# Optimization experiments

Measured on AMD Instinct MI355X. Metric: run time of the kernel, lower is better.

## Reference

```python
import jax, jax.numpy as jnp
import numpy as np

N = 100000   # nodes
E = 800000   # edges
NC = 500     # category nodes
EC = 20000   # category relation edges
D = 64       # out_feats
HOUR_PERIOD = 6  # emb_mix('hour') uses time_period = 6


def l2norm(x):
    # torch F.normalize(p=2, dim=-1) with eps clamp
    return x / jnp.maximum(jnp.linalg.norm(x, axis=-1, keepdims=True), 1e-12)


def proj_transh(x, norm):
    # x - <x, norm> * norm  (per-row)
    return x - jnp.sum(x * norm, axis=-1, keepdims=True) * norm


def edge_softmax(score, dst, n):
    # softmax over incoming edges of each destination node
    m = jax.ops.segment_max(score, dst, num_segments=n)
    e = jnp.exp(score - m[dst])
    s = jax.ops.segment_sum(e, dst, num_segments=n)
    return e / s[dst]


def setup_inputs() -> dict:
    key = jax.random.key(0)
    ks = jax.random.split(key, 12)
    nfeat = jax.random.normal(ks[0], (N, D), dtype=jnp.float32)
    cat_embedding = jax.random.normal(ks[1], (NC, D), dtype=jnp.float32)
    src = jax.random.randint(ks[2], (E,), 0, N, dtype=jnp.int32)
    dst = jax.random.randint(ks[3], (E,), 0, N, dtype=jnp.int32)
    feats_type = jax.random.randint(ks[4], (E,), 0, 7, dtype=jnp.int32)
    hour_id = jax.random.randint(ks[5], (E,), 0, HOUR_PERIOD, dtype=jnp.int32)
    cat_src = jax.random.randint(ks[6], (EC,), 0, NC, dtype=jnp.int32)
    cat_dst = jax.random.randint(ks[7], (EC,), 0, NC, dtype=jnp.int32)
    # learned parameters (embeddings are L2-normalized at init, as in torch code)
    rel_emb = l2norm(jax.random.normal(ks[8], (7, D), dtype=jnp.float32))
    norm_emb = l2norm(jax.random.normal(ks[9], (7, D), dtype=jnp.float32))
    hour_emb = l2norm(jax.random.normal(ks[10], (25, D), dtype=jnp.float32))
    time_rel_w = jax.random.normal(ks[11], (D, D), dtype=jnp.float32) * (1.0 / np.sqrt(D))
    time_rel_b = jnp.zeros((D,), dtype=jnp.float32)
    return {
        "nfeat": nfeat, "cat_embedding": cat_embedding,
        "rel_emb": rel_emb, "norm_emb": norm_emb, "hour_emb": hour_emb,
        "time_rel_w": time_rel_w, "time_rel_b": time_rel_b,
        "src": src, "dst": dst, "feats_type": feats_type, "hour_id": hour_id,
        "cat_src": cat_src, "cat_dst": cat_dst,
    }


def reference(nfeat, cat_embedding, rel_emb, norm_emb, hour_emb,
              time_rel_w, time_rel_b,
              src, dst, feats_type, hour_id, cat_src, cat_dst):
    # ---- category relation graph (cat_emb_type='relation', cat_score_type='transe')
    h_c = cat_embedding[cat_src]                        # [EC, D]
    t_c = cat_embedding[cat_dst]                        # [EC, D]
    rel_c = rel_emb[6]                                  # [D]
    diff_c = h_c + rel_c - t_c
    score_c = jnp.exp(-jnp.sum(diff_c * diff_c, axis=1))  # [EC]
    a_c = edge_softmax(score_c, cat_dst, NC)
    cat_hid = jax.ops.segment_sum(h_c * a_c[:, None], cat_dst, num_segments=NC)

    # ---- main graph edge features
    rel = rel_emb[feats_type]                           # [E, D]
    norm = norm_emb[feats_type]                         # [E, D]
    time_norm = norm_emb[5]                             # [D] (type-5 for all edges)
    # time relation: mixed hour embedding -> linear -> L2 normalize
    last_h = (hour_id - 1 + HOUR_PERIOD) % HOUR_PERIOD
    next_h = (hour_id + 1) % HOUR_PERIOD
    mix = (hour_emb[last_h] + hour_emb[hour_id] + hour_emb[next_h]) / 3.0  # [E, D]
    time_rel = l2norm(mix @ time_rel_w.T + time_rel_b)  # [E, D]

    h = nfeat[src]                                      # [E, D]
    t = nfeat[dst]                                      # [E, D]
    # TransH score on relation hyperplane
    d1 = proj_transh(h, norm) + rel - proj_transh(t, norm)
    score = jnp.exp(-jnp.sum(d1 * d1, axis=1))
    # TransH score on time hyperplane
    d2 = proj_transh(h, time_norm[None, :]) + time_rel - proj_transh(t, time_norm[None, :])
    score_t = jnp.exp(-jnp.sum(d2 * d2, axis=1))
    fin_score = score * score_t                         # [E]

    a = edge_softmax(fin_score, dst, N)                 # [E]
    rst = jax.ops.segment_sum(h * a[:, None], dst, num_segments=N)  # [N, D]
    return rst, cat_hid
```

## Files before the change

### kernel.cpp

```cpp
#include <hip/hip_runtime.h>

#define D 64
#define HOUR_PERIOD 6
#define CAPM 40
#define CAPC 96
#define CSTR 8

__device__ __forceinline__ float bf2f(unsigned short u) {
    union { unsigned int i; float f; } v; v.i = ((unsigned int)u) << 16; return v.f;
}
__device__ __forceinline__ unsigned short f2bf(float f) {
    union { float fl; unsigned int i; } v; v.fl = f;
    unsigned int x = v.i;
    return (unsigned short)((x + 0x7fffu + ((x >> 16) & 1u)) >> 16);
}
__device__ __forceinline__ float4 ld4(const void* base, int idx4, int fp32) {
    if (fp32) return reinterpret_cast<const float4*>(base)[idx4];
    ushort4 u = reinterpret_cast<const ushort4*>(base)[idx4];
    return make_float4(bf2f(u.x), bf2f(u.y), bf2f(u.z), bf2f(u.w));
}
__device__ __forceinline__ float ld1(const void* base, int i, int fp32) {
    return fp32 ? reinterpret_cast<const float*>(base)[i]
                : bf2f(reinterpret_cast<const unsigned short*>(base)[i]);
}
__device__ __forceinline__ void ld8(const void* base, int row, int l, int f,
                                    float& h0, float& h1, float& h2, float& h3,
                                    float& h4, float& h5, float& h6, float& h7) {
    if (f) {
        const float4* p = reinterpret_cast<const float4*>(base) + row * 16 + l * 2;
        float4 u = p[0], v = p[1];
        h0 = u.x; h1 = u.y; h2 = u.z; h3 = u.w;
        h4 = v.x; h5 = v.y; h6 = v.z; h7 = v.w;
    } else {
        uint4 u = reinterpret_cast<const uint4*>(base)[row * 8 + l];
        h0 = bf2f((unsigned short)(u.x & 0xFFFFu)); h1 = bf2f((unsigned short)(u.x >> 16));
        h2 = bf2f((unsigned short)(u.y & 0xFFFFu)); h3 = bf2f((unsigned short)(u.y >> 16));
        h4 = bf2f((unsigned short)(u.z & 0xFFFFu)); h5 = bf2f((unsigned short)(u.z >> 16));
        h6 = bf2f((unsigned short)(u.w & 0xFFFFu)); h7 = bf2f((unsigned short)(u.w >> 16));
    }
}
__device__ __forceinline__ int detect_f(const void* rel_emb) {
    int lane = threadIdx.x & 63;
    float da = bf2f(reinterpret_cast<const unsigned short*>(rel_emb)[lane]);
    float db = bf2f(reinterpret_cast<const unsigned short*>(rel_emb)[lane + 64]);
    int bad = (!(fabsf(da) <= 100.f)) || (!(fabsf(db) <= 100.f));
    unsigned long long m = __ballot(bad);
    return (m != 0ull) ? 1 : 0;
}
__device__ __forceinline__ float wsum64(float v) {
    #pragma unroll
    for (int off = 32; off; off >>= 1) v += __shfl_xor(v, off, 64);
    return v;
}
__device__ __forceinline__ float rsum8(float v) {
    v += __shfl_xor(v, 1, 64);
    v += __shfl_xor(v, 2, 64);
    v += __shfl_xor(v, 4, 64);
    return v;
}

__global__ void k_pp(const int* __restrict__ src, const int* __restrict__ dst,
                     const int* __restrict__ ft, const int* __restrict__ hh,
                     const int* __restrict__ csrc, const int* __restrict__ cdst,
                     int* __restrict__ cnt, unsigned* __restrict__ recsM,
                     unsigned* __restrict__ recsC,
                     const void* __restrict__ nfeat, const void* __restrict__ cemb,
                     const void* __restrict__ rel_emb, const void* __restrict__ norm_emb,
                     const void* __restrict__ hour_emb, const void* __restrict__ trw,
                     const void* __restrict__ trb,
                     unsigned* __restrict__ pmain, float2* __restrict__ pcat,
                     float* __restrict__ consts,
                     int E, int EC, int N, int NC, int GPREP) {
    __shared__ float vt[20 * D];
    __shared__ float mix6[HOUR_PERIOD * D];
    int t = threadIdx.x;
    if (blockIdx.x >= GPREP) {
        int tid = (blockIdx.x - GPREP) * 256 + t;
        if (tid < E) {
            int sv = src[tid], dv = dst[tid], fv = ft[tid], hv = hh[tid];
            int r = atomicAdd(&cnt[dv * CSTR], 1);
            if (r < CAPM)
                recsM[dv * CAPM + r] =
                    (unsigned)sv | ((unsigned)fv << 17) | ((unsigned)hv << 20);
        } else if (tid - E < EC) {
            int k = tid - E;
            int sv = csrc[k], dv = cdst[k];
            int r = atomicAdd(&cnt[(N + dv) * CSTR], 1);
            if (r < CAPC) recsC[dv * CAPC + r] = (unsigned)sv;
        }
        return;
    }
    int pb = blockIdx.x;
    int f = detect_f(rel_emb);
    int lane = t & 63, w = t >> 6;
    for (int i = t; i < 7 * D; i += 256) vt[i] = ld1(rel_emb, i, f);
    for (int i = t; i < 7 * D; i += 256) vt[7 * D + i] = ld1(norm_emb, i, f);
    for (int i = t; i < HOUR_PERIOD * D; i += 256) {
        int hv = i >> 6, k = i & 63;
        int last = (hv + HOUR_PERIOD - 1) % HOUR_PERIOD, next = (hv + 1) % HOUR_PERIOD;
        mix6[i] = (ld1(hour_emb, last * D + k, f) + ld1(hour_emb, hv * D + k, f) +
                   ld1(hour_emb, next * D + k, f)) * (1.f / 3.f);
    }
    __syncthreads();
    for (int hv = w; hv < HOUR_PERIOD; hv += 4) {
        float y = ld1(trb, lane, f);
        #pragma unroll 4
        for (int kk = 0; kk < D; ++kk)
            y += mix6[hv * D + kk] * ld1(trw, lane * D + kk, f);
        float ss = wsum64(y * y);
        vt[(14 + hv) * D + lane] = y / fmaxf(sqrtf(ss), 1e-12f);
    }
    __syncthreads();
    int tid = pb * 256 + t;
    if (tid < N) {
        float R0 = 0.f, R1 = 0.f, R2a = 0.f, R3 = 0.f, R4 = 0.f, R5 = 0.f, R6 = 0.f;
        float Nm0 = 0.f, Nm1 = 0.f, Nm2 = 0.f, Nm3 = 0.f, Nm4 = 0.f, Nm5 = 0.f, Nm6 = 0.f;
        float T0 = 0.f, T1 = 0.f, T2 = 0.f, T3 = 0.f, T4 = 0.f, T5 = 0.f;
        float S2 = 0.f;
        const float4* vp = reinterpret_cast<const float4*>(vt);
        #pragma unroll 2
        for (int k4 = 0; k4 < 16; ++k4) {
            float4 x = ld4(nfeat, tid * 16 + k4, f);
            #define DOTV(acc, v) { float4 qv = vp[(v) * 16 + k4]; \
                acc += x.x * qv.x + x.y * qv.y + x.z * qv.z + x.w * qv.w; }
            DOTV(R0, 0)  DOTV(R1, 1)  DOTV(R2a, 2) DOTV(R3, 3)
            DOTV(R4, 4)  DOTV(R5, 5)  DOTV(R6, 6)
            DOTV(Nm0, 7) DOTV(Nm1, 8) DOTV(Nm2, 9) DOTV(Nm3, 10)
            DOTV(Nm4, 11) DOTV(Nm5, 12) DOTV(Nm6, 13)
            DOTV(T0, 14) DOTV(T1, 15) DOTV(T2, 16) DOTV(T3, 17)
            DOTV(T4, 18) DOTV(T5, 19)
            #undef DOTV
            S2 += x.x * x.x + x.y * x.y + x.z * x.z + x.w * x.w;
        }
        unsigned w0 = (unsigned)f2bf(Nm0) | ((unsigned)f2bf(R0) << 16);
        unsigned w1 = (unsigned)f2bf(Nm1) | ((unsigned)f2bf(R1) << 16);
        unsigned w2 = (unsigned)f2bf(Nm2) | ((unsigned)f2bf(R2a) << 16);
        unsigned w3 = (unsigned)f2bf(Nm3) | ((unsigned)f2bf(R3) << 16);
        unsigned w4 = (unsigned)f2bf(Nm4) | ((unsigned)f2bf(R4) << 16);
        unsigned w5 = (unsigned)f2bf(Nm5) | ((unsigned)f2bf(R5) << 16);
        unsigned w6 = (unsigned)f2bf(Nm6) | ((unsigned)f2bf(R6) << 16);
        unsigned w7 = (unsigned)f2bf(T0) | ((unsigned)f2bf(T1) << 16);
        unsigned w8 = (unsigned)f2bf(T2) | ((unsigned)f2bf(T3) << 16);
        unsigned w9 = (unsigned)f2bf(T4) | ((unsigned)f2bf(T5) << 16);
        union { float ff; unsigned u; } cs, ca;
        cs.ff = S2; ca.ff = Nm5;
        uint4* dp = reinterpret_cast<uint4*>(pmain + (size_t)tid * 16);
        dp[0] = make_uint4(w0, w1, w2, w3);
        dp[1] = make_uint4(w4, w5, w6, w7);
        dp[2] = make_uint4(w8, w9, cs.u, ca.u);
        dp[3] = make_uint4(0, 0, 0, 0);
    } else if (tid - N < NC) {
        int i = tid - N;
        float S = 0.f, Cr = 0.f;
        #pragma unroll 4
        for (int k4 = 0; k4 < 16; ++k4) {
            float4 x = ld4(cemb, i * 16 + k4, f);
            float4 rv = *reinterpret_cast<const float4*>(&vt[6 * D + k4 * 4]);
            S  += x.x * x.x + x.y * x.y + x.z * x.z + x.w * x.w;
            Cr += x.x * rv.x + x.y * rv.y + x.z * rv.z + x.w * rv.w;
        }
        pcat[i] = make_float2(S, Cr);
    }
    if (pb == 0) {
        if (t < 7) {
            float R2 = 0.f, RN = 0.f, N2 = 0.f;
            for (int k = 0; k < D; ++k) {
                float r = vt[t * D + k], n = vt[(7 + t) * D + k];
                R2 += r * r; RN += r * n; N2 += n * n;
            }
            consts[t * 4 + 0] = R2; consts[t * 4 + 1] = RN;
            consts[t * 4 + 2] = N2 - 2.f; consts[t * 4 + 3] = 0.f;
        } else if (t < 13) {
            int hv = t - 7;
            float T2c = 0.f, TQ = 0.f;
            for (int k = 0; k < D; ++k) {
                float a = vt[(14 + hv) * D + k], qv = vt[12 * D + k];
                T2c += a * a; TQ += a * qv;
            }
            consts[28 + hv * 2] = T2c; consts[29 + hv * 2] = TQ;
        } else if (t == 13) {
            float Q2 = 0.f;
            for (int k = 0; k < D; ++k) { float qv = vt[12 * D + k]; Q2 += qv * qv; }
            consts[40] = Q2 - 2.f;
        } else if (t == 14) {
            float R = 0.f;
            for (int k = 0; k < D; ++k) { float r = vt[6 * D + k]; R += r * r; }
            consts[41] = R;
        }
    }
}

__launch_bounds__(256, 8)
__global__ void k_fused(const void* __restrict__ nfeat, const void* __restrict__ cemb,
                        const void* __restrict__ rel_emb,
                        const unsigned char* __restrict__ pmain,
                        const float2* __restrict__ pcat,
                        const float* __restrict__ consts,
                        const int* __restrict__ cnt,
                        const unsigned* __restrict__ recsM,
                        const unsigned* __restrict__ recsC,
                        void* __restrict__ out, int N, int M) {
    int t = threadIdx.x;
    int f = detect_f(rel_emb);
    __shared__ __align__(16) float sc[44];
    if (t < 42) sc[t] = consts[t];
    __syncthreads();
    int lane = t & 63, w = t >> 6;
    int l = lane & 7, q = lane >> 3;
    int d = blockIdx.x * 4 + w;
    if (d >= M) return;
    float Q2m2 = sc[40], R2c = sc[41];
    float a0 = 0.f, a1 = 0.f, a2 = 0.f, a3 = 0.f;
    float a4 = 0.f, a5 = 0.f, a6 = 0.f, a7 = 0.f, se = 0.f;
    if (d < N) {
        int i0 = d * CAPM;
        int nE = cnt[d * CSTR];
        unsigned pk = recsM[i0 + q];
        float t0, t1, t2, t3, t4, t5, t6, t7;
        ld8(nfeat, d, l, f, t0, t1, t2, t3, t4, t5, t6, t7);
        const unsigned char* pd = pmain + (size_t)d * 64;
        float2 sd2 = *reinterpret_cast<const float2*>(pd + 40);
        nE = nE > CAPM ? CAPM : nE;
        for (int b = 0; b < nE; b += 8) {
            unsigned pkn = 0u;
            if (b + 8 < nE) pkn = recsM[i0 + b + 8 + q];
            int valid = (b + q) < nE;
            unsigned pkv = valid ? pk : 0u;
            int s = pkv & 0x1FFFF, fv = (pkv >> 17) & 7, hv = (pkv >> 20) & 7;
            const unsigned char* ps = pmain + (size_t)s * 64;
            float h0, h1, h2, h3, h4, h5, h6, h7;
            ld8(nfeat, s, l, f, h0, h1, h2, h3, h4, h5, h6, h7);
            unsigned aws = *reinterpret_cast<const unsigned*>(ps + 4 * fv);
            unsigned short dhs = *reinterpret_cast<const unsigned short*>(ps + 28 + 2 * hv);
            float2 sa = *reinterpret_cast<const float2*>(ps + 40);
            unsigned awd = *reinterpret_cast<const unsigned*>(pd + 4 * fv);
            unsigned short dhd = *reinterpret_cast<const unsigned short*>(pd + 28 + 2 * hv);
            float4 cf  = *reinterpret_cast<float4*>(&sc[fv * 4]);
            float2 cth = *reinterpret_cast<float2*>(&sc[28 + hv * 2]);
            float hdot = rsum8(h0 * t0 + h1 * t1 + h2 * t2 + h3 * t3 +
                               h4 * t4 + h5 * t5 + h6 * t6 + h7 * t7);
            float As = bf2f((unsigned short)(aws & 0xFFFFu));
            float Cs = bf2f((unsigned short)(aws >> 16));
            float Ad = bf2f((unsigned short)(awd & 0xFFFFu));
            float Cd = bf2f((unsigned short)(awd >> 16));
            float Dhs = bf2f(dhs), Dhd = bf2f(dhd);
            float al = As - Ad;
            float be = sa.y - sd2.y;
            float w2 = sa.x + sd2.x - 2.f * hdot;
            float ssq = 2.f * w2 + cf.x + cth.x + 2.f * (Cs - Cd) + 2.f * (Dhs - Dhd)
                      + al * al * cf.z - 2.f * al * cf.y
                      + be * be * Q2m2 - 2.f * be * cth.y;
            float es = __expf(__expf(-ssq));
            es = valid ? es : 0.f;
            a0 += es * h0; a1 += es * h1; a2 += es * h2; a3 += es * h3;
            a4 += es * h4; a5 += es * h5; a6 += es * h6; a7 += es * h7;
            se += es;
            pk = pkn;
        }
    } else {
        int dc = d - N;
        int i0 = dc * CAPC;
        int nE = cnt[d * CSTR];
        unsigned pk = recsC[i0 + q];
        float t0, t1, t2, t3, t4, t5, t6, t7;
        ld8(cemb, dc, l, f, t0, t1, t2, t3, t4, t5, t6, t7);
        float2 td = pcat[dc];
        nE = nE > CAPC ? CAPC : nE;
        for (int b = 0; b < nE; b += 8) {
            unsigned pkn = 0u;
            if (b + 8 < nE) pkn = recsC[i0 + b + 8 + q];
            int valid = (b + q) < nE;
            unsigned s = valid ? pk : 0u;
            float h0, h1, h2, h3, h4, h5, h6, h7;
            ld8(cemb, (int)s, l, f, h0, h1, h2, h3, h4, h5, h6, h7);
            float2 csh = pcat[s];
            float hdot = rsum8(h0 * t0 + h1 * t1 + h2 * t2 + h3 * t3 +
                               h4 * t4 + h5 * t5 + h6 * t6 + h7 * t7);
            float ssq = csh.x + td.x + R2c + 2.f * csh.y - 2.f * td.y - 2.f * hdot;
            float es = __expf(__expf(-ssq));
            es = valid ? es : 0.f;
            a0 += es * h0; a1 += es * h1; a2 += es * h2; a3 += es * h3;
            a4 += es * h4; a5 += es * h5; a6 += es * h6; a7 += es * h7;
            se += es;
            pk = pkn;
        }
    }
    #define RED(x) x += __shfl_xor(x, 8, 64); x += __shfl_xor(x, 16, 64); x += __shfl_xor(x, 32, 64);
    RED(a0) RED(a1) RED(a2) RED(a3) RED(a4) RED(a5) RED(a6) RED(a7) RED(se)
    #undef RED
    float inv = (se > 0.f) ? 1.f / se : 0.f;
    if (q == 0) {
        if (f) {
            float4* op = reinterpret_cast<float4*>(out) + d * 16 + l * 2;
            op[0] = make_float4(a0 * inv, a1 * inv, a2 * inv, a3 * inv);
            op[1] = make_float4(a4 * inv, a5 * inv, a6 * inv, a7 * inv);
        } else {
            unsigned w0 = (unsigned)f2bf(a0 * inv) | ((unsigned)f2bf(a1 * inv) << 16);
            unsigned w1 = (unsigned)f2bf(a2 * inv) | ((unsigned)f2bf(a3 * inv) << 16);
            unsigned w2 = (unsigned)f2bf(a4 * inv) | ((unsigned)f2bf(a5 * inv) << 16);
            unsigned w3 = (unsigned)f2bf(a6 * inv) | ((unsigned)f2bf(a7 * inv) << 16);
            reinterpret_cast<uint4*>(out)[d * 8 + l] = make_uint4(w0, w1, w2, w3);
        }
    }
}

extern "C" void kernel_launch(void* const* d_in, const int* in_sizes, int n_in,
                              void* d_out, int out_size, void* d_ws, size_t ws_size,
                              hipStream_t stream) {
    const void* nfeat    = d_in[0];
    const void* cemb     = d_in[1];
    const void* rel_emb  = d_in[2];
    const void* norm_emb = d_in[3];
    const void* hour_emb = d_in[4];
    const void* trw      = d_in[5];
    const void* trb      = d_in[6];
    const int* src    = (const int*)d_in[7];
    const int* dst    = (const int*)d_in[8];
    const int* ftype  = (const int*)d_in[9];
    const int* hourid = (const int*)d_in[10];
    const int* csrc   = (const int*)d_in[11];
    const int* cdst   = (const int*)d_in[12];

    const int N  = in_sizes[0] / D;
    const int NC = in_sizes[1] / D;
    const int E  = in_sizes[7];
    const int EC = in_sizes[11];
    const int M  = N + NC;

    unsigned char* base = (unsigned char*)d_ws;
    size_t o = 0;
    int* cnt = (int*)(base + o);          o += ((size_t)M * CSTR * 4 + 255) & ~(size_t)255;
    float* consts = (float*)(base + o);   o += 256;
    unsigned* pmain = (unsigned*)(base + o); o += (size_t)N * 64;
    float2* pcat = (float2*)(base + o);   o += ((size_t)NC * 8 + 255) & ~(size_t)255;
    unsigned* recsM = (unsigned*)(base + o); o += (size_t)N * CAPM * 4;
    unsigned* recsC = (unsigned*)(base + o); o += (size_t)NC * CAPC * 4;

    (void)hipMemsetAsync(cnt, 0, (size_t)M * CSTR * 4, stream);

    int GP    = (E + EC + 255) / 256;
    int GPREP = (M + 255) / 256;
    k_pp<<<GPREP + GP, 256, 0, stream>>>(src, dst, ftype, hourid, csrc, cdst,
                                         cnt, recsM, recsC,
                                         nfeat, cemb, rel_emb, norm_emb,
                                         hour_emb, trw, trb,
                                         pmain, pcat, consts,
                                         E, EC, N, NC, GPREP);
    k_fused<<<(M + 3) / 4, 256, 0, stream>>>(nfeat, cemb, rel_emb,
                                             (const unsigned char*)pmain, pcat,
                                             consts, cnt,
                                             recsM, recsC, d_out, N, M);
}
```

Baseline: 213.3 us.

## Merge preprocessing and aggregation kernels into one persistent kernel with grid barrier

Replaces the two kernel launches with a single persistent kernel sized to the device's occupancy. Blocks grid-stride over the preprocessing and bucketing units, meet at a global atomic barrier, then grid-stride over destination nodes for aggregation. This removes one launch and the gap between kernels. In exchange, every block waits for the slowest block at the barrier, and the per-unit table setup now runs in every prep unit a block handles. The barrier deadlocks if the grid is larger than what can be co-resident on the device.

```diff
diff --git a/kernel.cpp b/kernel.cpp
--- a/kernel.cpp
+++ b/kernel.cpp
@@ -59,247 +59,253 @@
     return v;
 }
 
-__global__ void k_pp(const int* __restrict__ src, const int* __restrict__ dst,
-                     const int* __restrict__ ft, const int* __restrict__ hh,
-                     const int* __restrict__ csrc, const int* __restrict__ cdst,
-                     int* __restrict__ cnt, unsigned* __restrict__ recsM,
-                     unsigned* __restrict__ recsC,
-                     const void* __restrict__ nfeat, const void* __restrict__ cemb,
-                     const void* __restrict__ rel_emb, const void* __restrict__ norm_emb,
-                     const void* __restrict__ hour_emb, const void* __restrict__ trw,
-                     const void* __restrict__ trb,
-                     unsigned* __restrict__ pmain, float2* __restrict__ pcat,
-                     float* __restrict__ consts,
-                     int E, int EC, int N, int NC, int GPREP) {
+__global__ __launch_bounds__(256, 8) void k_mega(
+        const int* __restrict__ src, const int* __restrict__ dst,
+        const int* __restrict__ ft, const int* __restrict__ hh,
+        const int* __restrict__ csrc, const int* __restrict__ cdst,
+        int* __restrict__ cnt, unsigned* __restrict__ recsM,
+        unsigned* __restrict__ recsC,
+        const void* __restrict__ nfeat, const void* __restrict__ cemb,
+        const void* __restrict__ rel_emb, const void* __restrict__ norm_emb,
+        const void* __restrict__ hour_emb, const void* __restrict__ trw,
+        const void* __restrict__ trb,
+        unsigned* __restrict__ pmain, float2* __restrict__ pcat,
+        float* __restrict__ consts, int* __restrict__ bar,
+        void* __restrict__ out,
+        int E, int EC, int N, int NC, int M, int GPREP, int GP, int GRID) {
     __shared__ float vt[20 * D];
     __shared__ float mix6[HOUR_PERIOD * D];
+    __shared__ __align__(16) float sc[44];
     int t = threadIdx.x;
-    if (blockIdx.x >= GPREP) {
-        int tid = (blockIdx.x - GPREP) * 256 + t;
-        if (tid < E) {
-            int sv = src[tid], dv = dst[tid], fv = ft[tid], hv = hh[tid];
-            int r = atomicAdd(&cnt[dv * CSTR], 1);
-            if (r < CAPM)
-                recsM[dv * CAPM + r] =
-                    (unsigned)sv | ((unsigned)fv << 17) | ((unsigned)hv << 20);
-        } else if (tid - E < EC) {
-            int k = tid - E;
-            int sv = csrc[k], dv = cdst[k];
-            int r = atomicAdd(&cnt[(N + dv) * CSTR], 1);
-            if (r < CAPC) recsC[dv * CAPC + r] = (unsigned)sv;
-        }
-        return;
-    }
-    int pb = blockIdx.x;
     int f = detect_f(rel_emb);
     int lane = t & 63, w = t >> 6;
-    for (int i = t; i < 7 * D; i += 256) vt[i] = ld1(rel_emb, i, f);
-    for (int i = t; i < 7 * D; i += 256) vt[7 * D + i] = ld1(norm_emb, i, f);
-    for (int i = t; i < HOUR_PERIOD * D; i += 256) {
-        int hv = i >> 6, k = i & 63;
-        int last = (hv + HOUR_PERIOD - 1) % HOUR_PERIOD, next = (hv + 1) % HOUR_PERIOD;
-        mix6[i] = (ld1(hour_emb, last * D + k, f) + ld1(hour_emb, hv * D + k, f) +
-                   ld1(hour_emb, next * D + k, f)) * (1.f / 3.f);
-    }
+
+    int nunits = GPREP + GP;
+    for (int u = blockIdx.x; u < nunits; u += GRID) {
+        if (u < GPREP) {
+            for (int i = t; i < 7 * D; i += 256) vt[i] = ld1(rel_emb, i, f);
+            for (int i = t; i < 7 * D; i += 256) vt[7 * D + i] = ld1(norm_emb, i, f);
+            for (int i = t; i < HOUR_PERIOD * D; i += 256) {
+                int hv = i >> 6, k = i & 63;
+                int last = (hv + HOUR_PERIOD - 1) % HOUR_PERIOD, next = (hv + 1) % HOUR_PERIOD;
+                mix6[i] = (ld1(hour_emb, last * D + k, f) + ld1(hour_emb, hv * D + k, f) +
+                           ld1(hour_emb, next * D + k, f)) * (1.f / 3.f);
+            }
+            __syncthreads();
+            for (int hv = w; hv < HOUR_PERIOD; hv += 4) {
+                float y = ld1(trb, lane, f);
+                #pragma unroll 4
+                for (int kk = 0; kk < D; ++kk)
+                    y += mix6[hv * D + kk] * ld1(trw, lane * D + kk, f);
+                float ss = wsum64(y * y);
+                vt[(14 + hv) * D + lane] = y / fmaxf(sqrtf(ss), 1e-12f);
+            }
+            __syncthreads();
+            int tid = u * 256 + t;
+            if (tid < N) {
+                float R0 = 0.f, R1 = 0.f, R2a = 0.f, R3 = 0.f, R4 = 0.f, R5 = 0.f, R6 = 0.f;
+                float Nm0 = 0.f, Nm1 = 0.f, Nm2 = 0.f, Nm3 = 0.f, Nm4 = 0.f, Nm5 = 0.f, Nm6 = 0.f;
+                float T0 = 0.f, T1 = 0.f, T2 = 0.f, T3 = 0.f, T4 = 0.f, T5 = 0.f;
+                float S2 = 0.f;
+                const float4* vp = reinterpret_cast<const float4*>(vt);
+                #pragma unroll 2
+                for (int k4 = 0; k4 < 16; ++k4) {
+                    float4 x = ld4(nfeat, tid * 16 + k4, f);
+                    #define DOTV(acc, v) { float4 qv = vp[(v) * 16 + k4]; \
+                        acc += x.x * qv.x + x.y * qv.y + x.z * qv.z + x.w * qv.w; }
+                    DOTV(R0, 0)  DOTV(R1, 1)  DOTV(R2a, 2) DOTV(R3, 3)
+                    DOTV(R4, 4)  DOTV(R5, 5)  DOTV(R6, 6)
+                    DOTV(Nm0, 7) DOTV(Nm1, 8) DOTV(Nm2, 9) DOTV(Nm3, 10)
+                    DOTV(Nm4, 11) DOTV(Nm5, 12) DOTV(Nm6, 13)
+                    DOTV(T0, 14) DOTV(T1, 15) DOTV(T2, 16) DOTV(T3, 17)
+                    DOTV(T4, 18) DOTV(T5, 19)
+                    #undef DOTV
+                    S2 += x.x * x.x + x.y * x.y + x.z * x.z + x.w * x.w;
+                }
+                unsigned w0 = (unsigned)f2bf(Nm0) | ((unsigned)f2bf(R0) << 16);
+                unsigned w1 = (unsigned)f2bf(Nm1) | ((unsigned)f2bf(R1) << 16);
+                unsigned w2 = (unsigned)f2bf(Nm2) | ((unsigned)f2bf(R2a) << 16);
+                unsigned w3 = (unsigned)f2bf(Nm3) | ((unsigned)f2bf(R3) << 16);
+                unsigned w4 = (unsigned)f2bf(Nm4) | ((unsigned)f2bf(R4) << 16);
+                unsigned w5 = (unsigned)f2bf(Nm5) | ((unsigned)f2bf(R5) << 16);
+                unsigned w6 = (unsigned)f2bf(Nm6) | ((unsigned)f2bf(R6) << 16);
+                unsigned w7 = (unsigned)f2bf(T0) | ((unsigned)f2bf(T1) << 16);
+                unsigned w8 = (unsigned)f2bf(T2) | ((unsigned)f2bf(T3) << 16);
+                unsigned w9 = (unsigned)f2bf(T4) | ((unsigned)f2bf(T5) << 16);
+                union { float ff; unsigned u32; } cs, ca;
+                cs.ff = S2; ca.ff = Nm5;
+                uint4* dp = reinterpret_cast<uint4*>(pmain + (size_t)tid * 16);
+                dp[0] = make_uint4(w0, w1, w2, w3);
+                dp[1] = make_uint4(w4, w5, w6, w7);
+                dp[2] = make_uint4(w8, w9, cs.u32, ca.u32);
+                dp[3] = make_uint4(0, 0, 0, 0);
+            } else if (tid - N < NC) {
+                int i = tid - N;
+                float S = 0.f, Cr = 0.f;
+                #pragma unroll 4
+                for (int k4 = 0; k4 < 16; ++k4) {
+                    float4 x = ld4(cemb, i * 16 + k4, f);
+                    float4 rv = *reinterpret_cast<const float4*>(&vt[6 * D + k4 * 4]);
+                    S  += x.x * x.x + x.y * x.y + x.z * x.z + x.w * x.w;
+                    Cr += x.x * rv.x + x.y * rv.y + x.z * rv.z + x.w * rv.w;
+                }
+                pcat[i] = make_float2(S, Cr);
+            }
+            if (u == 0) {
+                if (t < 7) {
+                    float R2 = 0.f, RN = 0.f, N2 = 0.f;
+                    for (int k = 0; k < D; ++k) {
+                        float r = vt[t * D + k], n = vt[(7 + t) * D + k];
+                        R2 += r * r; RN += r * n; N2 += n * n;
+                    }
+                    consts[t * 4 + 0] = R2; consts[t * 4 + 1] = RN;
+                    consts[t * 4 + 2] = N2 - 2.f; consts[t * 4 + 3] = 0.f;
+                } else if (t < 13) {
+                    int hv = t - 7;
+                    float T2c = 0.f, TQ = 0.f;
+                    for (int k = 0; k < D; ++k) {
+                        float a = vt[(14 + hv) * D + k], qv = vt[12 * D + k];
+                        T2c += a * a; TQ += a * qv;
+                    }
+                    consts[28 + hv * 2] = T2c; consts[29 + hv * 2] = TQ;
+                } else if (t == 13) {
+                    float Q2 = 0.f;
+                    for (int k = 0; k < D; ++k) { float qv = vt[12 * D + k]; Q2 += qv * qv; }
+                    consts[40] = Q2 - 2.f;
+                } else if (t == 14) {
+                    float R = 0.f;
+                    for (int k = 0; k < D; ++k) { float r = vt[6 * D + k]; R += r * r; }
+                    consts[41] = R;
+                }
+            }
+            __syncthreads();
+        } else {
+            int tid = (u - GPREP) * 256 + t;
+            if (tid < E) {
+                int sv = src[tid], dv = dst[tid], fv = ft[tid], hv = hh[tid];
+                int r = atomicAdd(&cnt[dv * CSTR], 1);
+                if (r < CAPM)
+                    recsM[dv * CAPM + r] =
+                        (unsigned)sv | ((unsigned)fv << 17) | ((unsigned)hv << 20);
+            } else if (tid - E < EC) {
+                int k = tid - E;
+                int sv = csrc[k], dv = cdst[k];
+                int r = atomicAdd(&cnt[(N + dv) * CSTR], 1);
+                if (r < CAPC) recsC[dv * CAPC + r] = (unsigned)sv;
+            }
+        }
+    }
+
     __syncthreads();
-    for (int hv = w; hv < HOUR_PERIOD; hv += 4) {
-        float y = ld1(trb, lane, f);
-        #pragma unroll 4
-        for (int kk = 0; kk < D; ++kk)
-            y += mix6[hv * D + kk] * ld1(trw, lane * D + kk, f);
-        float ss = wsum64(y * y);
-        vt[(14 + hv) * D + lane] = y / fmaxf(sqrtf(ss), 1e-12f);
+    if (t == 0) {
+        __hip_atomic_fetch_add(bar, 1, __ATOMIC_RELEASE, __HIP_MEMORY_SCOPE_AGENT);
+        #pragma unroll 1
+        for (int it = 0;; ++it) {
+            if (__hip_atomic_load(bar, __ATOMIC_RELAXED, __HIP_MEMORY_SCOPE_AGENT) >= GRID)
+                break;
+            if (it < 32) __builtin_amdgcn_s_sleep(2);
+            else         __builtin_amdgcn_s_sleep(64);
+        }
+        (void)__hip_atomic_load(bar, __ATOMIC_ACQUIRE, __HIP_MEMORY_SCOPE_AGENT);
     }
     __syncthreads();
-    int tid = pb * 256 + t;
-    if (tid < N) {
-        float R0 = 0.f, R1 = 0.f, R2a = 0.f, R3 = 0.f, R4 = 0.f, R5 = 0.f, R6 = 0.f;
-        float Nm0 = 0.f, Nm1 = 0.f, Nm2 = 0.f, Nm3 = 0.f, Nm4 = 0.f, Nm5 = 0.f, Nm6 = 0.f;
-        float T0 = 0.f, T1 = 0.f, T2 = 0.f, T3 = 0.f, T4 = 0.f, T5 = 0.f;
-        float S2 = 0.f;
-        const float4* vp = reinterpret_cast<const float4*>(vt);
-        #pragma unroll 2
-        for (int k4 = 0; k4 < 16; ++k4) {
-            float4 x = ld4(nfeat, tid * 16 + k4, f);
-            #define DOTV(acc, v) { float4 qv = vp[(v) * 16 + k4]; \
-                acc += x.x * qv.x + x.y * qv.y + x.z * qv.z + x.w * qv.w; }
-            DOTV(R0, 0)  DOTV(R1, 1)  DOTV(R2a, 2) DOTV(R3, 3)
-            DOTV(R4, 4)  DOTV(R5, 5)  DOTV(R6, 6)
-            DOTV(Nm0, 7) DOTV(Nm1, 8) DOTV(Nm2, 9) DOTV(Nm3, 10)
-            DOTV(Nm4, 11) DOTV(Nm5, 12) DOTV(Nm6, 13)
-            DOTV(T0, 14) DOTV(T1, 15) DOTV(T2, 16) DOTV(T3, 17)
-            DOTV(T4, 18) DOTV(T5, 19)
-            #undef DOTV
-            S2 += x.x * x.x + x.y * x.y + x.z * x.z + x.w * x.w;
-        }
-        unsigned w0 = (unsigned)f2bf(Nm0) | ((unsigned)f2bf(R0) << 16);
-        unsigned w1 = (unsigned)f2bf(Nm1) | ((unsigned)f2bf(R1) << 16);
-        unsigned w2 = (unsigned)f2bf(Nm2) | ((unsigned)f2bf(R2a) << 16);
-        unsigned w3 = (unsigned)f2bf(Nm3) | ((unsigned)f2bf(R3) << 16);
-        unsigned w4 = (unsigned)f2bf(Nm4) | ((unsigned)f2bf(R4) << 16);
-        unsigned w5 = (unsigned)f2bf(Nm5) | ((unsigned)f2bf(R5) << 16);
-        unsigned w6 = (unsigned)f2bf(Nm6) | ((unsigned)f2bf(R6) << 16);
-        unsigned w7 = (unsigned)f2bf(T0) | ((unsigned)f2bf(T1) << 16);
-        unsigned w8 = (unsigned)f2bf(T2) | ((unsigned)f2bf(T3) << 16);
-        unsigned w9 = (unsigned)f2bf(T4) | ((unsigned)f2bf(T5) << 16);
-        union { float ff; unsigned u; } cs, ca;
-        cs.ff = S2; ca.ff = Nm5;
-        uint4* dp = reinterpret_cast<uint4*>(pmain + (size_t)tid * 16);
-        dp[0] = make_uint4(w0, w1, w2, w3);
-        dp[1] = make_uint4(w4, w5, w6, w7);
-        dp[2] = make_uint4(w8, w9, cs.u, ca.u);
-        dp[3] = make_uint4(0, 0, 0, 0);
-    } else if (tid - N < NC) {
-        int i = tid - N;
-        float S = 0.f, Cr = 0.f;
-        #pragma unroll 4
-        for (int k4 = 0; k4 < 16; ++k4) {
-            float4 x = ld4(cemb, i * 16 + k4, f);
-            float4 rv = *reinterpret_cast<const float4*>(&vt[6 * D + k4 * 4]);
-            S  += x.x * x.x + x.y * x.y + x.z * x.z + x.w * x.w;
-            Cr += x.x * rv.x + x.y * rv.y + x.z * rv.z + x.w * rv.w;
-        }
-        pcat[i] = make_float2(S, Cr);
-    }
-    if (pb == 0) {
-        if (t < 7) {
-            float R2 = 0.f, RN = 0.f, N2 = 0.f;
-            for (int k = 0; k < D; ++k) {
-                float r = vt[t * D + k], n = vt[(7 + t) * D + k];
-                R2 += r * r; RN += r * n; N2 += n * n;
-            }
-            consts[t * 4 + 0] = R2; consts[t * 4 + 1] = RN;
-            consts[t * 4 + 2] = N2 - 2.f; consts[t * 4 + 3] = 0.f;
-        } else if (t < 13) {
-            int hv = t - 7;
-            float T2c = 0.f, TQ = 0.f;
-            for (int k = 0; k < D; ++k) {
-                float a = vt[(14 + hv) * D + k], qv = vt[12 * D + k];
-                T2c += a * a; TQ += a * qv;
-            }
-            consts[28 + hv * 2] = T2c; consts[29 + hv * 2] = TQ;
-        } else if (t == 13) {
-            float Q2 = 0.f;
-            for (int k = 0; k < D; ++k) { float qv = vt[12 * D + k]; Q2 += qv * qv; }
-            consts[40] = Q2 - 2.f;
-        } else if (t == 14) {
-            float R = 0.f;
-            for (int k = 0; k < D; ++k) { float r = vt[6 * D + k]; R += r * r; }
-            consts[41] = R;
-        }
-    }
-}
-
-__launch_bounds__(256, 8)
-__global__ void k_fused(const void* __restrict__ nfeat, const void* __restrict__ cemb,
-                        const void* __restrict__ rel_emb,
-                        const unsigned char* __restrict__ pmain,
-                        const float2* __restrict__ pcat,
-                        const float* __restrict__ consts,
-                        const int* __restrict__ cnt,
-                        const unsigned* __restrict__ recsM,
-                        const unsigned* __restrict__ recsC,
-                        void* __restrict__ out, int N, int M) {
-    int t = threadIdx.x;
-    int f = detect_f(rel_emb);
-    __shared__ __align__(16) float sc[44];
+
     if (t < 42) sc[t] = consts[t];
     __syncthreads();
-    int lane = t & 63, w = t >> 6;
     int l = lane & 7, q = lane >> 3;
-    int d = blockIdx.x * 4 + w;
-    if (d >= M) return;
     float Q2m2 = sc[40], R2c = sc[41];
-    float a0 = 0.f, a1 = 0.f, a2 = 0.f, a3 = 0.f;
-    float a4 = 0.f, a5 = 0.f, a6 = 0.f, a7 = 0.f, se = 0.f;
-    if (d < N) {
-        int i0 = d * CAPM;
-        int nE = cnt[d * CSTR];
-        unsigned pk = recsM[i0 + q];
-        float t0, t1, t2, t3, t4, t5, t6, t7;
-        ld8(nfeat, d, l, f, t0, t1, t2, t3, t4, t5, t6, t7);
-        const unsigned char* pd = pmain + (size_t)d * 64;
-        float2 sd2 = *reinterpret_cast<const float2*>(pd + 40);
-        nE = nE > CAPM ? CAPM : nE;
-        for (int b = 0; b < nE; b += 8) {
-            unsigned pkn = 0u;
-            if (b + 8 < nE) pkn = recsM[i0 + b + 8 + q];
-            int valid = (b + q) < nE;
-            unsigned pkv = valid ? pk : 0u;
-            int s = pkv & 0x1FFFF, fv = (pkv >> 17) & 7, hv = (pkv >> 20) & 7;
-            const unsigned char* ps = pmain + (size_t)s * 64;
-            float h0, h1, h2, h3, h4, h5, h6, h7;
-            ld8(nfeat, s, l, f, h0, h1, h2, h3, h4, h5, h6, h7);
-            unsigned aws = *reinterpret_cast<const unsigned*>(ps + 4 * fv);
-            unsigned short dhs = *reinterpret_cast<const unsigned short*>(ps + 28 + 2 * hv);
-            float2 sa = *reinterpret_cast<const float2*>(ps + 40);
-            unsigned awd = *reinterpret_cast<const unsigned*>(pd + 4 * fv);
-            unsigned short dhd = *reinterpret_cast<const unsigned short*>(pd + 28 + 2 * hv);
-            float4 cf  = *reinterpret_cast<float4*>(&sc[fv * 4]);
-            float2 cth = *reinterpret_cast<float2*>(&sc[28 + hv * 2]);
-            float hdot = rsum8(h0 * t0 + h1 * t1 + h2 * t2 + h3 * t3 +
-                               h4 * t4 + h5 * t5 + h6 * t6 + h7 * t7);
-            float As = bf2f((unsigned short)(aws & 0xFFFFu));
-            float Cs = bf2f((unsigned short)(aws >> 16));
-            float Ad = bf2f((unsigned short)(awd & 0xFFFFu));
-            float Cd = bf2f((unsigned short)(awd >> 16));
-            float Dhs = bf2f(dhs), Dhd = bf2f(dhd);
-            float al = As - Ad;
-            float be = sa.y - sd2.y;
-            float w2 = sa.x + sd2.x - 2.f * hdot;
-            float ssq = 2.f * w2 + cf.x + cth.x + 2.f * (Cs - Cd) + 2.f * (Dhs - Dhd)
-                      + al * al * cf.z - 2.f * al * cf.y
-                      + be * be * Q2m2 - 2.f * be * cth.y;
-            float es = __expf(__expf(-ssq));
-            es = valid ? es : 0.f;
-            a0 += es * h0; a1 += es * h1; a2 += es * h2; a3 += es * h3;
-            a4 += es * h4; a5 += es * h5; a6 += es * h6; a7 += es * h7;
-            se += es;
-            pk = pkn;
+    for (int d = blockIdx.x * 4 + w; d < M; d += GRID * 4) {
+        float a0 = 0.f, a1 = 0.f, a2 = 0.f, a3 = 0.f;
+        float a4 = 0.f, a5 = 0.f, a6 = 0.f, a7 = 0.f, se = 0.f;
+        if (d < N) {
+            int i0 = d * CAPM;
+            int nE = cnt[d * CSTR];
+            unsigned pk = recsM[i0 + q];
+            float t0, t1, t2, t3, t4, t5, t6, t7;
+            ld8(nfeat, d, l, f, t0, t1, t2, t3, t4, t5, t6, t7);
+            const unsigned char* pd = reinterpret_cast<const unsigned char*>(pmain) + (size_t)d * 64;
+            float2 sd2 = *reinterpret_cast<const float2*>(pd + 40);
+            nE = nE > CAPM ? CAPM : nE;
+            for (int b = 0; b < nE; b += 8) {
+                unsigned pkn = 0u;
+                if (b + 8 < nE) pkn = recsM[i0 + b + 8 + q];
+                int valid = (b + q) < nE;
+                unsigned pkv = valid ? pk : 0u;
+                int s = pkv & 0x1FFFF, fv = (pkv >> 17) & 7, hv = (pkv >> 20) & 7;
+                const unsigned char* ps = reinterpret_cast<const unsigned char*>(pmain) + (size_t)s * 64;
+                float h0, h1, h2, h3, h4, h5, h6, h7;
+                ld8(nfeat, s, l, f, h0, h1, h2, h3, h4, h5, h6, h7);
+                unsigned aws = *reinterpret_cast<const unsigned*>(ps + 4 * fv);
+                unsigned short dhs = *reinterpret_cast<const unsigned short*>(ps + 28 + 2 * hv);
+                float2 sa = *reinterpret_cast<const float2*>(ps + 40);
+                unsigned awd = *reinterpret_cast<const unsigned*>(pd + 4 * fv);
+                unsigned short dhd = *reinterpret_cast<const unsigned short*>(pd + 28 + 2 * hv);
+                float4 cf  = *reinterpret_cast<float4*>(&sc[fv * 4]);
+                float2 cth = *reinterpret_cast<float2*>(&sc[28 + hv * 2]);
+                float hdot = rsum8(h0 * t0 + h1 * t1 + h2 * t2 + h3 * t3 +
+                                   h4 * t4 + h5 * t5 + h6 * t6 + h7 * t7);
+                float As = bf2f((unsigned short)(aws & 0xFFFFu));
+                float Cs = bf2f((unsigned short)(aws >> 16));
+                float Ad = bf2f((unsigned short)(awd & 0xFFFFu));
+                float Cd = bf2f((unsigned short)(awd >> 16));
+                float Dhs = bf2f(dhs), Dhd = bf2f(dhd);
+                float al = As - Ad;
+                float be = sa.y - sd2.y;
+                float w2 = sa.x + sd2.x - 2.f * hdot;
+                float ssq = 2.f * w2 + cf.x + cth.x + 2.f * (Cs - Cd) + 2.f * (Dhs - Dhd)
+                          + al * al * cf.z - 2.f * al * cf.y
+                          + be * be * Q2m2 - 2.f * be * cth.y;
+                float es = __expf(__expf(-ssq));
+                es = valid ? es : 0.f;
+                a0 += es * h0; a1 += es * h1; a2 += es * h2; a3 += es * h3;
+                a4 += es * h4; a5 += es * h5; a6 += es * h6; a7 += es * h7;
+                se += es;
+                pk = pkn;
+            }
+        } else {
+            int dc = d - N;
+            int i0 = dc * CAPC;
+            int nE = cnt[d * CSTR];
+            unsigned pk = recsC[i0 + q];
+            float t0, t1, t2, t3, t4, t5, t6, t7;
+            ld8(cemb, dc, l, f, t0, t1, t2, t3, t4, t5, t6, t7);
+            float2 td = pcat[dc];
+            nE = nE > CAPC ? CAPC : nE;
+            for (int b = 0; b < nE; b += 8) {
+                unsigned pkn = 0u;
+                if (b + 8 < nE) pkn = recsC[i0 + b + 8 + q];
+                int valid = (b + q) < nE;
+                unsigned s = valid ? pk : 0u;
+                float h0, h1, h2, h3, h4, h5, h6, h7;
+                ld8(cemb, (int)s, l, f, h0, h1, h2, h3, h4, h5, h6, h7);
+                float2 csh = pcat[s];
+                float hdot = rsum8(h0 * t0 + h1 * t1 + h2 * t2 + h3 * t3 +
+                                   h4 * t4 + h5 * t5 + h6 * t6 + h7 * t7);
+                float ssq = csh.x + td.x + R2c + 2.f * csh.y - 2.f * td.y - 2.f * hdot;
+                float es = __expf(__expf(-ssq));
+                es = valid ? es : 0.f;
+                a0 += es * h0; a1 += es * h1; a2 += es * h2; a3 += es * h3;
+                a4 += es * h4; a5 += es * h5; a6 += es * h6; a7 += es * h7;
+                se += es;
+                pk = pkn;
+            }
         }
-    } else {
-        int dc = d - N;
-        int i0 = dc * CAPC;
-        int nE = cnt[d * CSTR];
-        unsigned pk = recsC[i0 + q];
-        float t0, t1, t2, t3, t4, t5, t6, t7;
-        ld8(cemb, dc, l, f, t0, t1, t2, t3, t4, t5, t6, t7);
-        float2 td = pcat[dc];
-        nE = nE > CAPC ? CAPC : nE;
-        for (int b = 0; b < nE; b += 8) {
-            unsigned pkn = 0u;
-            if (b + 8 < nE) pkn = recsC[i0 + b + 8 + q];
-            int valid = (b + q) < nE;
-            unsigned s = valid ? pk : 0u;
-            float h0, h1, h2, h3, h4, h5, h6, h7;
-            ld8(cemb, (int)s, l, f, h0, h1, h2, h3, h4, h5, h6, h7);
-            float2 csh = pcat[s];
-            float hdot = rsum8(h0 * t0 + h1 * t1 + h2 * t2 + h3 * t3 +
-                               h4 * t4 + h5 * t5 + h6 * t6 + h7 * t7);
-            float ssq = csh.x + td.x + R2c + 2.f * csh.y - 2.f * td.y - 2.f * hdot;
-            float es = __expf(__expf(-ssq));
-            es = valid ? es : 0.f;
-            a0 += es * h0; a1 += es * h1; a2 += es * h2; a3 += es * h3;
-            a4 += es * h4; a5 += es * h5; a6 += es * h6; a7 += es * h7;
-            se += es;
-            pk = pkn;
-        }
-    }
-    #define RED(x) x += __shfl_xor(x, 8, 64); x += __shfl_xor(x, 16, 64); x += __shfl_xor(x, 32, 64);
-    RED(a0) RED(a1) RED(a2) RED(a3) RED(a4) RED(a5) RED(a6) RED(a7) RED(se)
-    #undef RED
-    float inv = (se > 0.f) ? 1.f / se : 0.f;
-    if (q == 0) {
-        if (f) {
-            float4* op = reinterpret_cast<float4*>(out) + d * 16 + l * 2;
-            op[0] = make_float4(a0 * inv, a1 * inv, a2 * inv, a3 * inv);
-            op[1] = make_float4(a4 * inv, a5 * inv, a6 * inv, a7 * inv);
-        } else {
-            unsigned w0 = (unsigned)f2bf(a0 * inv) | ((unsigned)f2bf(a1 * inv) << 16);
-            unsigned w1 = (unsigned)f2bf(a2 * inv) | ((unsigned)f2bf(a3 * inv) << 16);
-            unsigned w2 = (unsigned)f2bf(a4 * inv) | ((unsigned)f2bf(a5 * inv) << 16);
-            unsigned w3 = (unsigned)f2bf(a6 * inv) | ((unsigned)f2bf(a7 * inv) << 16);
-            reinterpret_cast<uint4*>(out)[d * 8 + l] = make_uint4(w0, w1, w2, w3);
+        #define RED(x) x += __shfl_xor(x, 8, 64); x += __shfl_xor(x, 16, 64); x += __shfl_xor(x, 32, 64);
+        RED(a0) RED(a1) RED(a2) RED(a3) RED(a4) RED(a5) RED(a6) RED(a7) RED(se)
+        #undef RED
+        float inv = (se > 0.f) ? 1.f / se : 0.f;
+        if (q == 0) {
+            if (f) {
+                float4* op = reinterpret_cast<float4*>(out) + d * 16 + l * 2;
+                op[0] = make_float4(a0 * inv, a1 * inv, a2 * inv, a3 * inv);
+                op[1] = make_float4(a4 * inv, a5 * inv, a6 * inv, a7 * inv);
+            } else {
+                unsigned w0 = (unsigned)f2bf(a0 * inv) | ((unsigned)f2bf(a1 * inv) << 16);
+                unsigned w1 = (unsigned)f2bf(a2 * inv) | ((unsigned)f2bf(a3 * inv) << 16);
+                unsigned w2 = (unsigned)f2bf(a4 * inv) | ((unsigned)f2bf(a5 * inv) << 16);
+                unsigned w3 = (unsigned)f2bf(a6 * inv) | ((unsigned)f2bf(a7 * inv) << 16);
+                reinterpret_cast<uint4*>(out)[d * 8 + l] = make_uint4(w0, w1, w2, w3);
+            }
         }
     }
 }
@@ -327,8 +333,24 @@
     const int EC = in_sizes[11];
     const int M  = N + NC;
 
+    static int g_grid = -1;
+    if (g_grid < 0) {
+        int nb = 0;
+        if (hipOccupancyMaxActiveBlocksPerMultiprocessor(&nb, k_mega, 256, 0) != hipSuccess
+            || nb <= 0) nb = 4;
+        int cu = 256;
+        static hipDeviceProp_t prop;
+        if (hipGetDeviceProperties(&prop, 0) == hipSuccess && prop.multiProcessorCount > 0)
+            cu = prop.multiProcessorCount;
+        long g = (long)nb * cu;
+        if (g > 4096) g = 4096;
+        if (g < 64) g = 64;
+        g_grid = (int)g;
+    }
+
     unsigned char* base = (unsigned char*)d_ws;
     size_t o = 0;
+    int* bar = (int*)(base + o);          o += 256;
     int* cnt = (int*)(base + o);          o += ((size_t)M * CSTR * 4 + 255) & ~(size_t)255;
     float* consts = (float*)(base + o);   o += 256;
     unsigned* pmain = (unsigned*)(base + o); o += (size_t)N * 64;
@@ -336,18 +358,14 @@
     unsigned* recsM = (unsigned*)(base + o); o += (size_t)N * CAPM * 4;
     unsigned* recsC = (unsigned*)(base + o); o += (size_t)NC * CAPC * 4;
 
-    (void)hipMemsetAsync(cnt, 0, (size_t)M * CSTR * 4, stream);
+    (void)hipMemsetAsync(base, 0, 256 + (((size_t)M * CSTR * 4 + 255) & ~(size_t)255), stream);
 
     int GP    = (E + EC + 255) / 256;
     int GPREP = (M + 255) / 256;
-    k_pp<<<GPREP + GP, 256, 0, stream>>>(src, dst, ftype, hourid, csrc, cdst,
-                                         cnt, recsM, recsC,
-                                         nfeat, cemb, rel_emb, norm_emb,
-                                         hour_emb, trw, trb,
-                                         pmain, pcat, consts,
-                                         E, EC, N, NC, GPREP);
-    k_fused<<<(M + 3) / 4, 256, 0, stream>>>(nfeat, cemb, rel_emb,
-                                             (const unsigned char*)pmain, pcat,
-                                             consts, cnt,
-                                             recsM, recsC, d_out, N, M);
-}
+    k_mega<<<g_grid, 256, 0, stream>>>(src, dst, ftype, hourid, csrc, cdst,
+                                       cnt, recsM, recsC,
+                                       nfeat, cemb, rel_emb, norm_emb,
+                                       hour_emb, trw, trb,
+                                       pmain, pcat, consts, bar, d_out,
+                                       E, EC, N, NC, M, GPREP, GP, g_grid);
+}
```

New measurement: 461.1 us. 2.16x slower.
